# Kernel tuning notes

Measured on AMD Instinct MI355X. Metric: run time of the kernel, lower is better.

## Reference

```python
import jax, jax.numpy as jnp
import numpy as np

B, S, H, NH = 4, 2048, 512, 8
HD = H // NH  # head dim = 64


def setup_inputs() -> dict:
    key = jax.random.key(0)
    ks = jax.random.split(key, 12)
    f = lambda k, sh: jax.random.normal(k, sh, dtype=jnp.float32)
    w = lambda k: f(k, (H, H)) * 0.02  # Linear weight (out, in), torch-style
    return {
        "q": f(ks[0], (B, S, H)),
        "k": f(ks[1], (B, S, H)),
        "v": f(ks[2], (B, S, H)),
        "mask": jax.random.randint(ks[3], (B, S, S), 0, 2, dtype=jnp.int32),
        "Wq": w(ks[4]), "bq": jnp.zeros((H,), jnp.float32),
        "Wk": w(ks[5]), "bk": jnp.zeros((H,), jnp.float32),
        "Wv": w(ks[6]), "bv": jnp.zeros((H,), jnp.float32),
        "Wo": w(ks[7]), "bo": jnp.zeros((H,), jnp.float32),
    }


def reference(q, k, v, mask, Wq, bq, Wk, bk, Wv, bv, Wo, bo):
    b, s, h = q.shape
    scale = jnp.asarray(np.sqrt(HD), q.dtype)
    # QKV projections (torch Linear: x @ W.T + b), split into heads: b n s h
    def heads(x, W, bias):
        y = x @ W.T + bias
        return y.reshape(b, s, NH, HD).transpose(0, 2, 1, 3)
    Q = heads(q, Wq, bq)
    K = heads(k, Wk, bk)
    V = heads(v, Wv, bv)
    scores = jnp.einsum('bnsh,bnth->bnst', Q, K) / scale
    scores = jnp.where(mask[:, None, :, :] == 0, jnp.asarray(-1e9, scores.dtype), scores)
    attn = jax.nn.softmax(scores, axis=-1)
    # dropout is identity in eval mode
    out = jnp.einsum('bnst,bnth->bnsh', attn, V)
    out = out.transpose(0, 2, 1, 3).reshape(b, s, h)
    return out @ Wo.T + bo
```

## Files before the change

### kernel.cpp

```cpp
#include <hip/hip_runtime.h>
#include <cstdint>


typedef __bf16 bf16x8 __attribute__((ext_vector_type(8)));
typedef float  f32x4  __attribute__((ext_vector_type(4)));
typedef float  f32x16 __attribute__((ext_vector_type(16)));

#define MFMA16(a, b, c) __builtin_amdgcn_mfma_f32_16x16x32_bf16(a, b, c, 0, 0, 0)
#define MFMA32(a, b, c) __builtin_amdgcn_mfma_f32_32x32x16_bf16(a, b, c, 0, 0, 0)

__device__ __forceinline__ ushort f2bf(float f) {
  union { __bf16 h; ushort u; } v; v.h = (__bf16)f; return v.u;
}

typedef const __attribute__((address_space(1))) unsigned int* gas_u32;
typedef __attribute__((address_space(3))) unsigned int* las_u32;
__device__ __forceinline__ void gll16(const void* g, void* l) {
  __builtin_amdgcn_global_load_lds((gas_u32)g, (las_u32)l, 16, 0, 0);
}

__global__ __launch_bounds__(256) void cvt_bf16(
    const float* __restrict__ src, ushort* __restrict__ dst, int n4) {
  int i = blockIdx.x * 256 + threadIdx.x;
  int stride = gridDim.x * 256;
  for (; i < n4; i += stride) {
    float4 v = ((const float4*)src)[i];
    ushort4 o = { f2bf(v.x), f2bf(v.y), f2bf(v.z), f2bf(v.w) };
    ((ushort4*)dst)[i] = o;
  }
}

__global__ __launch_bounds__(256) void cvt_w(
    const float* __restrict__ w0, const float* __restrict__ w1,
    const float* __restrict__ w2, const float* __restrict__ w3,
    ushort* __restrict__ dst) {
  const float* src = (blockIdx.y == 0) ? w0 : (blockIdx.y == 1) ? w1
                   : (blockIdx.y == 2) ? w2 : w3;
  ushort* d = dst + (size_t)blockIdx.y * 262144;
  int i = blockIdx.x * 256 + threadIdx.x;
  for (int j = i; j < 65536; j += 16384) {
    float4 v = ((const float4*)src)[j];
    ushort4 o = { f2bf(v.x), f2bf(v.y), f2bf(v.z), f2bf(v.w) };
    ((ushort4*)d)[j] = o;
  }
}

__global__ __launch_bounds__(256) void mask_bits_kernel(
    const int* __restrict__ mask, unsigned long long* __restrict__ MB) {
  const int lane = threadIdx.x & 63;
  const int wv = (int)((blockIdx.x * 256 + threadIdx.x) >> 6);
  const size_t base = (size_t)wv * 64;
  for (int j = 0; j < 64; j += 4) {
    int v0 = mask[(base + j + 0) * 64 + lane];
    int v1 = mask[(base + j + 1) * 64 + lane];
    int v2 = mask[(base + j + 2) * 64 + lane];
    int v3 = mask[(base + j + 3) * 64 + lane];
    unsigned long long b0 = __ballot(v0 != 0), b1 = __ballot(v1 != 0);
    unsigned long long b2 = __ballot(v2 != 0), b3 = __ballot(v3 != 0);
    if (lane == 0) {
      MB[base + j] = b0; MB[base + j + 1] = b1;
      MB[base + j + 2] = b2; MB[base + j + 3] = b3;
    }
  }
}

template <int EPI>
__global__ __launch_bounds__(256) void gemm_bt16(
    const ushort* __restrict__ X, const ushort* __restrict__ W,
    const float* __restrict__ bias, void* __restrict__ Y, float scale) {
  __shared__ ushort As[64 * 64];
  __shared__ ushort Ws[128 * 64];
  const int tid = threadIdx.x, wv = tid >> 6, l = tid & 63;
  const int quad = l >> 4, ln = l & 15;
  const int m0 = blockIdx.x * 64, n0 = blockIdx.y * 128;
  const int wm = (wv & 1) * 32, wn = (wv >> 1) * 64;
  const int sr = l >> 3, sc = l & 7;
  f32x4 acc[2][4] = {};
  for (int kk = 0; kk < 512; kk += 64) {
#pragma unroll
    for (int i = 0; i < 2; ++i) {
      int row = wv * 16 + i * 8 + sr;
      gll16(X + (size_t)(m0 + row) * 512 + kk + ((sc ^ (row & 7)) * 8),
            As + (wv * 16 + i * 8) * 64);
    }
#pragma unroll
    for (int i = 0; i < 4; ++i) {
      int row = wv * 32 + i * 8 + sr;
      gll16(W + (size_t)(n0 + row) * 512 + kk + ((sc ^ (row & 7)) * 8),
            Ws + (wv * 32 + i * 8) * 64);
    }
    __syncthreads();
#pragma unroll
    for (int ks = 0; ks < 2; ++ks) {
      bf16x8 a[2], bw[4];
#pragma unroll
      for (int mt = 0; mt < 2; ++mt) {
        int row = wm + mt * 16 + ln;
        a[mt] = *(const bf16x8*)&As[row * 64 + (((ks * 4 + quad) ^ (row & 7)) * 8)];
      }
#pragma unroll
      for (int nt = 0; nt < 4; ++nt) {
        int row = wn + nt * 16 + ln;
        bw[nt] = *(const bf16x8*)&Ws[row * 64 + (((ks * 4 + quad) ^ (row & 7)) * 8)];
      }
#pragma unroll
      for (int mt = 0; mt < 2; ++mt)
#pragma unroll
        for (int nt = 0; nt < 4; ++nt)
          acc[mt][nt] = MFMA16(a[mt], bw[nt], acc[mt][nt]);
    }
    __syncthreads();
  }
  float bval[4];
#pragma unroll
  for (int nt = 0; nt < 4; ++nt) bval[nt] = bias[n0 + wn + nt * 16 + ln];

  if constexpr (EPI == 1) {
#pragma unroll
    for (int nt = 0; nt < 4; ++nt) {
      int row = wn + nt * 16 + ln;
#pragma unroll
      for (int mt = 0; mt < 2; ++mt) {
        int mbase = wm + mt * 16 + quad * 4;
        ushort4 pk;
        pk.x = f2bf(acc[mt][nt][0] + bval[nt]);
        pk.y = f2bf(acc[mt][nt][1] + bval[nt]);
        pk.z = f2bf(acc[mt][nt][2] + bval[nt]);
        pk.w = f2bf(acc[mt][nt][3] + bval[nt]);
        int col = ((mbase >> 3) ^ (row & 7)) * 8 + ((mbase >> 2) & 1) * 4;
        *(ushort4*)&Ws[row * 64 + col] = pk;
      }
    }
    __syncthreads();
#pragma unroll
    for (int i = 0; i < 4; ++i) {
      int c = tid + i * 256;
      int row = c >> 3, cs = c & 7;
      int cl = cs ^ (row & 7);
      uint4 d = *(const uint4*)&Ws[row * 64 + cs * 8];
      int n = n0 + row, m = m0 + cl * 8;
      int bb = m >> 11, s = m & 2047, h = n >> 6, hd = n & 63;
      *(uint4*)((ushort*)Y + ((size_t)((bb * 8 + h) * 64 + hd)) * 2048 + s) = d;
    }
  } else {
#pragma unroll
    for (int mt = 0; mt < 2; ++mt)
#pragma unroll
      for (int nt = 0; nt < 4; ++nt) {
        int n = n0 + wn + nt * 16 + ln;
#pragma unroll
        for (int r = 0; r < 4; ++r) {
          int m = m0 + wm + mt * 16 + quad * 4 + r;
          float val = (acc[mt][nt][r] + bval[nt]) * scale;
          if constexpr (EPI == 0) {
            int bb = m >> 11, s = m & 2047, h = n >> 6, hd = n & 63;
            ((ushort*)Y)[(((size_t)(bb * 8 + h) * 2048) + s) * 64 + hd] = f2bf(val);
          } else {
            ((float*)Y)[(size_t)m * 512 + n] = val;
          }
        }
      }
  }
}

__global__ __launch_bounds__(256, 4) void attn(
    const ushort* __restrict__ Qh, const ushort* __restrict__ Kh,
    const ushort* __restrict__ Vt, const unsigned long long* __restrict__ MB,
    ushort* __restrict__ O) {
  __shared__ ushort SMEM[16384];
  ushort* Ks = SMEM;
  ushort* Vs = SMEM + 8192;
  const int tid = threadIdx.x, wv = tid >> 6, lane = tid & 63;
  const int hs = lane >> 5, lq = lane & 31;
  const int qh = wv >> 1, kvh = wv & 1;
  const int bh = blockIdx.x, qb = blockIdx.y;
  const size_t hoff = (size_t)bh * 2048 * 64;
  const int q0 = qb * 64;
  const int qg = q0 + qh * 32 + lq;
  const int srK = lane >> 3, scK = lane & 7;
  const int srV = lane >> 4, scV = lane & 15;

  bf16x8 qf[4];
#pragma unroll
  for (int ki = 0; ki < 4; ++ki)
    qf[ki] = *(const bf16x8*)(Qh + hoff + (size_t)qg * 64 + ki * 16 + hs * 8);

  f32x16 po0 = {}, po1 = {};
  float l_own = 0.f;
  const unsigned long long* mrow = MB + ((size_t)(bh >> 3) * 2048 + qg) * 32;

  for (int it = 0; it < 16; ++it) {
    const int kv0 = it * 128;
#pragma unroll
    for (int i = 0; i < 4; ++i) {
      int row = wv * 32 + i * 8 + srK;
      gll16(Kh + hoff + (size_t)(kv0 + row) * 64 + ((scK ^ (row & 7)) * 8),
            Ks + (wv * 32 + i * 8) * 64);
      int rv = wv * 16 + i * 4 + srV;
      gll16(Vt + hoff + (size_t)rv * 2048 + kv0 + ((scV ^ (rv & 7)) * 8),
            Vs + (wv * 16 + i * 4) * 128);
    }
    unsigned long long mbw = mrow[it * 2 + kvh];
    __syncthreads();

#pragma unroll
    for (int ch = 0; ch < 2; ++ch) {
      const int kvb = kvh * 64 + ch * 32;
      f32x16 sc_ = {};
#pragma unroll
      for (int ki = 0; ki < 4; ++ki) {
        int row = kvb + lq;
        bf16x8 ak = *(const bf16x8*)&Ks[row * 64 + (((2 * ki + hs) ^ (row & 7)) * 8)];
        sc_ = MFMA32(ak, qf[ki], sc_);
      }
      uint pk[8];
      float psum = 0.f;
#pragma unroll
      for (int c = 0; c < 4; ++c) {
        unsigned nib = (unsigned)(mbw >> (ch * 32 + c * 8 + hs * 4)) & 0xFu;
        float p0 = (nib & 1u) ? exp2f(sc_[4 * c + 0]) : 0.f;
        float p1 = (nib & 2u) ? exp2f(sc_[4 * c + 1]) : 0.f;
        float p2 = (nib & 4u) ? exp2f(sc_[4 * c + 2]) : 0.f;
        float p3 = (nib & 8u) ? exp2f(sc_[4 * c + 3]) : 0.f;
        psum += (p0 + p1) + (p2 + p3);
        pk[2 * c + 0] = (uint)f2bf(p0) | ((uint)f2bf(p1) << 16);
        pk[2 * c + 1] = (uint)f2bf(p2) | ((uint)f2bf(p3) << 16);
      }
      l_own += psum;
      uint bx[4];
#pragma unroll
      for (int t2 = 0; t2 < 2; ++t2)
#pragma unroll
        for (int b2 = 0; b2 < 2; ++b2) {
          uint snd = hs ? pk[4 * t2 + b2] : pk[4 * t2 + 2 + b2];
          bx[t2 * 2 + b2] = (uint)__shfl_xor((int)snd, 32);
        }
#pragma unroll
      for (int t2 = 0; t2 < 2; ++t2) {
        union { uint u[4]; bf16x8 v; } bp;
        bp.u[0] = hs ? bx[2 * t2 + 0] : pk[4 * t2 + 0];
        bp.u[1] = hs ? bx[2 * t2 + 1] : pk[4 * t2 + 1];
        bp.u[2] = hs ? pk[4 * t2 + 2] : bx[2 * t2 + 0];
        bp.u[3] = hs ? pk[4 * t2 + 3] : bx[2 * t2 + 1];
#pragma unroll
        for (int m2 = 0; m2 < 2; ++m2) {
          int hd = m2 * 32 + lq;
          int gch = (kvb >> 3) + 2 * t2 + hs;
          bf16x8 av = *(const bf16x8*)&Vs[hd * 128 + ((gch ^ (hd & 7)) * 8)];
          if (m2 == 0) po0 = MFMA32(av, bp.v, po0);
          else         po1 = MFMA32(av, bp.v, po1);
        }
      }
    }
    __syncthreads();
  }

  l_own += __shfl_xor(l_own, 32);
  float* psh = (float*)Ks;
  float* lsh = (float*)Vs;
  ushort* Osh = Vs + 256;
  if (kvh == 1) {
#pragma unroll
    for (int i = 0; i < 16; ++i) psh[(qh * 32 + i) * 64 + lane] = po0[i];
#pragma unroll
    for (int i = 0; i < 16; ++i) psh[(qh * 32 + 16 + i) * 64 + lane] = po1[i];
    lsh[qh * 64 + lane] = l_own;
  }
  __syncthreads();
  if (kvh == 0) {
    float linv = 1.0f / (l_own + lsh[qh * 64 + lane]);
    int row = qh * 32 + lq;
#pragma unroll
    for (int m2 = 0; m2 < 2; ++m2) {
#pragma unroll
      for (int c = 0; c < 4; ++c)
#pragma unroll
        for (int b2 = 0; b2 < 2; ++b2) {
          int r = 4 * c + 2 * b2;
          float v0, v1;
          if (m2 == 0) {
            v0 = (po0[r] + psh[(qh * 32 + r) * 64 + lane]) * linv;
            v1 = (po0[r + 1] + psh[(qh * 32 + r + 1) * 64 + lane]) * linv;
          } else {
            v0 = (po1[r] + psh[(qh * 32 + 16 + r) * 64 + lane]) * linv;
            v1 = (po1[r + 1] + psh[(qh * 32 + 16 + r + 1) * 64 + lane]) * linv;
          }
          int hd = m2 * 32 + 8 * c + 4 * hs + 2 * b2;
          *(uint*)&Osh[row * 72 + hd] = (uint)f2bf(v0) | ((uint)f2bf(v1) << 16);
        }
    }
  }
  __syncthreads();
  for (int i = tid; i < 512; i += 256) {
    int row = i >> 3, cc = i & 7;
    uint4 d = *(const uint4*)&Osh[row * 72 + cc * 8];
    *(uint4*)(O + ((size_t)((bh >> 3) * 2048 + q0 + row)) * 512 +
              (bh & 7) * 64 + cc * 8) = d;
  }
}

extern "C" void kernel_launch(void* const* d_in, const int* in_sizes, int n_in,
                              void* d_out, int out_size, void* d_ws, size_t ws_size,
                              hipStream_t stream) {
  const float* q    = (const float*)d_in[0];
  const float* k    = (const float*)d_in[1];
  const float* v    = (const float*)d_in[2];
  const int*   mask = (const int*)d_in[3];
  const float* Wq   = (const float*)d_in[4];
  const float* bq   = (const float*)d_in[5];
  const float* Wk   = (const float*)d_in[6];
  const float* bk   = (const float*)d_in[7];
  const float* Wv   = (const float*)d_in[8];
  const float* bv   = (const float*)d_in[9];
  const float* Wo   = (const float*)d_in[10];
  const float* bo   = (const float*)d_in[11];
  float* out = (float*)d_out;

  uint8_t* ws = (uint8_t*)d_ws;
  const size_t MiB = 1u << 20;
  ushort* Xb = (ushort*)(ws + 0 * MiB);
  ushort* Qh = (ushort*)(ws + 8 * MiB);
  ushort* Kh = (ushort*)(ws + 16 * MiB);
  ushort* Vt = (ushort*)(ws + 24 * MiB);
  unsigned long long* MB = (unsigned long long*)(ws + 32 * MiB);
  ushort* Wb = (ushort*)(ws + 34 * MiB);

  cvt_w<<<dim3(64, 4), 256, 0, stream>>>(Wq, Wk, Wv, Wo, Wb);
  mask_bits_kernel<<<1024, 256, 0, stream>>>(mask, MB);

  cvt_bf16<<<1024, 256, 0, stream>>>(q, Xb, 1048576);
  gemm_bt16<0><<<dim3(128, 4), 256, 0, stream>>>(Xb, Wb, bq, Qh, 0.18033688011112042f);
  cvt_bf16<<<1024, 256, 0, stream>>>(k, Xb, 1048576);
  gemm_bt16<0><<<dim3(128, 4), 256, 0, stream>>>(Xb, Wb + 262144, bk, Kh, 1.0f);
  cvt_bf16<<<1024, 256, 0, stream>>>(v, Xb, 1048576);
  gemm_bt16<1><<<dim3(128, 4), 256, 0, stream>>>(Xb, Wb + 2 * 262144, bv, Vt, 1.0f);

  attn<<<dim3(32, 32), 256, 0, stream>>>(Qh, Kh, Vt, MB, Xb);
  gemm_bt16<2><<<dim3(128, 4), 256, 0, stream>>>(Xb, Wb + 3 * 262144, bo, out, 1.0f);
}
```

Measured before the change: 285.7 us.

## Fuse fp32-to-bf16 conversion into batched QKV GEMM and register-prefetch attention K/V

Drops the three separate activation conversion kernels. A single batched QKV GEMM launch (grid z=3) loads fp32 activations straight into LDS and converts them to bf16 when reading MFMA fragments. This removes three kernel launches and the round trip of the bf16 activation buffer through memory. The attention loop now double-buffers K/V tiles and mask words in registers, loading the next tile while computing the current one, in place of direct global-to-LDS loads followed by a barrier. The cost is higher register pressure and doubled fp32 LDS traffic in the GEMM. The LDS writes also lose the XOR swizzle on the store side, so they depend on the global address swizzle matching.

New measurement: 542.0 us. 1.9x slower.

```diff
diff --git a/kernel.cpp b/kernel.cpp
--- a/kernel.cpp
+++ b/kernel.cpp
@@ -17,17 +17,6 @@
 typedef __attribute__((address_space(3))) unsigned int* las_u32;
 __device__ __forceinline__ void gll16(const void* g, void* l) {
   __builtin_amdgcn_global_load_lds((gas_u32)g, (las_u32)l, 16, 0, 0);
-}
-
-__global__ __launch_bounds__(256) void cvt_bf16(
-    const float* __restrict__ src, ushort* __restrict__ dst, int n4) {
-  int i = blockIdx.x * 256 + threadIdx.x;
-  int stride = gridDim.x * 256;
-  for (; i < n4; i += stride) {
-    float4 v = ((const float4*)src)[i];
-    ushort4 o = { f2bf(v.x), f2bf(v.y), f2bf(v.z), f2bf(v.w) };
-    ((ushort4*)dst)[i] = o;
-  }
 }
 
 __global__ __launch_bounds__(256) void cvt_w(
@@ -64,29 +53,37 @@
   }
 }
 
-template <int EPI>
-__global__ __launch_bounds__(256) void gemm_bt16(
-    const ushort* __restrict__ X, const ushort* __restrict__ W,
-    const float* __restrict__ bias, void* __restrict__ Y, float scale) {
-  __shared__ ushort As[64 * 64];
+__global__ __launch_bounds__(256) void qkv_gemm(
+    const float* __restrict__ q, const float* __restrict__ k,
+    const float* __restrict__ v, const ushort* __restrict__ Wb,
+    const float* __restrict__ bq, const float* __restrict__ bk,
+    const float* __restrict__ bv, ushort* __restrict__ Qh,
+    ushort* __restrict__ Kh, ushort* __restrict__ Vt) {
+  __shared__ float  Asf[64 * 64];
   __shared__ ushort Ws[128 * 64];
+  const int z = blockIdx.z;
+  const float* X = (z == 0) ? q : (z == 1) ? k : v;
+  const ushort* W = Wb + (size_t)z * 262144;
+  const float* bias = (z == 0) ? bq : (z == 1) ? bk : bv;
+  const float scale = (z == 0) ? 0.18033688011112042f : 1.0f;
+  ushort* Y = (z == 0) ? Qh : (z == 1) ? Kh : Vt;
+
   const int tid = threadIdx.x, wv = tid >> 6, l = tid & 63;
   const int quad = l >> 4, ln = l & 15;
   const int m0 = blockIdx.x * 64, n0 = blockIdx.y * 128;
   const int wm = (wv & 1) * 32, wn = (wv >> 1) * 64;
-  const int sr = l >> 3, sc = l & 7;
+  const int srA = l >> 4, sA = l & 15, cA = sA >> 1, hA = sA & 1;
+  const int srW = l >> 3, scW = l & 7;
   f32x4 acc[2][4] = {};
+
   for (int kk = 0; kk < 512; kk += 64) {
 #pragma unroll
-    for (int i = 0; i < 2; ++i) {
-      int row = wv * 16 + i * 8 + sr;
-      gll16(X + (size_t)(m0 + row) * 512 + kk + ((sc ^ (row & 7)) * 8),
-            As + (wv * 16 + i * 8) * 64);
-    }
-#pragma unroll
     for (int i = 0; i < 4; ++i) {
-      int row = wv * 32 + i * 8 + sr;
-      gll16(W + (size_t)(n0 + row) * 512 + kk + ((sc ^ (row & 7)) * 8),
+      int rowa = wv * 16 + i * 4 + srA;
+      gll16(X + (size_t)(m0 + rowa) * 512 + kk + ((cA ^ (rowa & 7)) * 8 + hA * 4),
+            Asf + (wv * 16 + i * 4) * 64);
+      int roww = wv * 32 + i * 8 + srW;
+      gll16(W + (size_t)(n0 + roww) * 512 + kk + ((scW ^ (roww & 7)) * 8),
             Ws + (wv * 32 + i * 8) * 64);
     }
     __syncthreads();
@@ -96,7 +93,14 @@
 #pragma unroll
       for (int mt = 0; mt < 2; ++mt) {
         int row = wm + mt * 16 + ln;
-        a[mt] = *(const bf16x8*)&As[row * 64 + (((ks * 4 + quad) ^ (row & 7)) * 8)];
+        int p = (ks * 4 + quad) ^ (row & 7);
+        const float* ap = &Asf[row * 64 + p * 8];
+        f32x4 x0 = *(const f32x4*)ap;
+        f32x4 x1 = *(const f32x4*)(ap + 4);
+        bf16x8 t;
+#pragma unroll
+        for (int j = 0; j < 4; ++j) { t[j] = (__bf16)x0[j]; t[4 + j] = (__bf16)x1[j]; }
+        a[mt] = t;
       }
 #pragma unroll
       for (int nt = 0; nt < 4; ++nt) {
@@ -115,7 +119,7 @@
 #pragma unroll
   for (int nt = 0; nt < 4; ++nt) bval[nt] = bias[n0 + wn + nt * 16 + ln];
 
-  if constexpr (EPI == 1) {
+  if (z == 2) {
 #pragma unroll
     for (int nt = 0; nt < 4; ++nt) {
       int row = wn + nt * 16 + ln;
@@ -140,7 +144,7 @@
       uint4 d = *(const uint4*)&Ws[row * 64 + cs * 8];
       int n = n0 + row, m = m0 + cl * 8;
       int bb = m >> 11, s = m & 2047, h = n >> 6, hd = n & 63;
-      *(uint4*)((ushort*)Y + ((size_t)((bb * 8 + h) * 64 + hd)) * 2048 + s) = d;
+      *(uint4*)(Y + ((size_t)((bb * 8 + h) * 64 + hd)) * 2048 + s) = d;
     }
   } else {
 #pragma unroll
@@ -152,12 +156,8 @@
         for (int r = 0; r < 4; ++r) {
           int m = m0 + wm + mt * 16 + quad * 4 + r;
           float val = (acc[mt][nt][r] + bval[nt]) * scale;
-          if constexpr (EPI == 0) {
-            int bb = m >> 11, s = m & 2047, h = n >> 6, hd = n & 63;
-            ((ushort*)Y)[(((size_t)(bb * 8 + h) * 2048) + s) * 64 + hd] = f2bf(val);
-          } else {
-            ((float*)Y)[(size_t)m * 512 + n] = val;
-          }
+          int bb = m >> 11, s = m & 2047, h = n >> 6, hd = n & 63;
+          Y[(((size_t)(bb * 8 + h) * 2048) + s) * 64 + hd] = f2bf(val);
         }
       }
   }
@@ -179,30 +179,59 @@
   const int qg = q0 + qh * 32 + lq;
   const int srK = lane >> 3, scK = lane & 7;
   const int srV = lane >> 4, scV = lane & 15;
+  const ushort* Kbase = Kh + hoff;
+  const ushort* Vbase = Vt + hoff;
 
   bf16x8 qf[4];
 #pragma unroll
   for (int ki = 0; ki < 4; ++ki)
     qf[ki] = *(const bf16x8*)(Qh + hoff + (size_t)qg * 64 + ki * 16 + hs * 8);
+
+  int lK[4], lV[4];
+  size_t gK[4], gV[4];
+#pragma unroll
+  for (int i = 0; i < 4; ++i) {
+    int rowK = wv * 32 + i * 8 + srK;
+    gK[i] = (size_t)rowK * 64 + ((scK ^ (rowK & 7)) * 8);
+    lK[i] = rowK * 64 + scK * 8;
+    int rowV = wv * 16 + i * 4 + srV;
+    gV[i] = (size_t)rowV * 2048 + ((scV ^ (rowV & 7)) * 8);
+    lV[i] = rowV * 128 + scV * 8;
+  }
 
   f32x16 po0 = {}, po1 = {};
   float l_own = 0.f;
   const unsigned long long* mrow = MB + ((size_t)(bh >> 3) * 2048 + qg) * 32;
 
+  uint4 kr[2][4], vr[2][4];
+  unsigned long long mb[2];
+#pragma unroll
+  for (int i = 0; i < 4; ++i) {
+    kr[0][i] = *(const uint4*)(Kbase + gK[i]);
+    vr[0][i] = *(const uint4*)(Vbase + gV[i]);
+  }
+  mb[0] = mrow[kvh];
+
+#pragma unroll 2
   for (int it = 0; it < 16; ++it) {
-    const int kv0 = it * 128;
+    const int p = it & 1;
 #pragma unroll
     for (int i = 0; i < 4; ++i) {
-      int row = wv * 32 + i * 8 + srK;
-      gll16(Kh + hoff + (size_t)(kv0 + row) * 64 + ((scK ^ (row & 7)) * 8),
-            Ks + (wv * 32 + i * 8) * 64);
-      int rv = wv * 16 + i * 4 + srV;
-      gll16(Vt + hoff + (size_t)rv * 2048 + kv0 + ((scV ^ (rv & 7)) * 8),
-            Vs + (wv * 16 + i * 4) * 128);
-    }
-    unsigned long long mbw = mrow[it * 2 + kvh];
-    __syncthreads();
-
+      *(uint4*)&Ks[lK[i]] = kr[p][i];
+      *(uint4*)&Vs[lV[i]] = vr[p][i];
+    }
+    if (it < 15) {
+      const size_t kvo = (size_t)(it + 1) * 128;
+#pragma unroll
+      for (int i = 0; i < 4; ++i) {
+        kr[p ^ 1][i] = *(const uint4*)(Kbase + kvo * 64 + gK[i]);
+        vr[p ^ 1][i] = *(const uint4*)(Vbase + kvo + gV[i]);
+      }
+      mb[p ^ 1] = mrow[(it + 1) * 2 + kvh];
+    }
+    __syncthreads();
+
+    const unsigned long long mbw = mb[p];
 #pragma unroll
     for (int ch = 0; ch < 2; ++ch) {
       const int kvb = kvh * 64 + ch * 32;
@@ -297,6 +326,66 @@
     *(uint4*)(O + ((size_t)((bh >> 3) * 2048 + q0 + row)) * 512 +
               (bh & 7) * 64 + cc * 8) = d;
   }
+}
+
+__global__ __launch_bounds__(256) void out_gemm(
+    const ushort* __restrict__ X, const ushort* __restrict__ W,
+    const float* __restrict__ bias, float* __restrict__ Y) {
+  __shared__ ushort As[64 * 64];
+  __shared__ ushort Ws[128 * 64];
+  const int tid = threadIdx.x, wv = tid >> 6, l = tid & 63;
+  const int quad = l >> 4, ln = l & 15;
+  const int m0 = blockIdx.x * 64, n0 = blockIdx.y * 128;
+  const int wm = (wv & 1) * 32, wn = (wv >> 1) * 64;
+  const int sr = l >> 3, sc = l & 7;
+  f32x4 acc[2][4] = {};
+  for (int kk = 0; kk < 512; kk += 64) {
+#pragma unroll
+    for (int i = 0; i < 2; ++i) {
+      int row = wv * 16 + i * 8 + sr;
+      gll16(X + (size_t)(m0 + row) * 512 + kk + ((sc ^ (row & 7)) * 8),
+            As + (wv * 16 + i * 8) * 64);
+    }
+#pragma unroll
+    for (int i = 0; i < 4; ++i) {
+      int row = wv * 32 + i * 8 + sr;
+      gll16(W + (size_t)(n0 + row) * 512 + kk + ((sc ^ (row & 7)) * 8),
+            Ws + (wv * 32 + i * 8) * 64);
+    }
+    __syncthreads();
+#pragma unroll
+    for (int ks = 0; ks < 2; ++ks) {
+      bf16x8 a[2], bw[4];
+#pragma unroll
+      for (int mt = 0; mt < 2; ++mt) {
+        int row = wm + mt * 16 + ln;
+        a[mt] = *(const bf16x8*)&As[row * 64 + (((ks * 4 + quad) ^ (row & 7)) * 8)];
+      }
+#pragma unroll
+      for (int nt = 0; nt < 4; ++nt) {
+        int row = wn + nt * 16 + ln;
+        bw[nt] = *(const bf16x8*)&Ws[row * 64 + (((ks * 4 + quad) ^ (row & 7)) * 8)];
+      }
+#pragma unroll
+      for (int mt = 0; mt < 2; ++mt)
+#pragma unroll
+        for (int nt = 0; nt < 4; ++nt)
+          acc[mt][nt] = MFMA16(a[mt], bw[nt], acc[mt][nt]);
+    }
+    __syncthreads();
+  }
+#pragma unroll
+  for (int mt = 0; mt < 2; ++mt)
+#pragma unroll
+    for (int nt = 0; nt < 4; ++nt) {
+      int n = n0 + wn + nt * 16 + ln;
+      float bval = bias[n];
+#pragma unroll
+      for (int r = 0; r < 4; ++r) {
+        int m = m0 + wm + mt * 16 + quad * 4 + r;
+        Y[(size_t)m * 512 + n] = acc[mt][nt][r] + bval;
+      }
+    }
 }
 
 extern "C" void kernel_launch(void* const* d_in, const int* in_sizes, int n_in,
@@ -318,7 +407,7 @@
 
   uint8_t* ws = (uint8_t*)d_ws;
   const size_t MiB = 1u << 20;
-  ushort* Xb = (ushort*)(ws + 0 * MiB);
+  ushort* Oh = (ushort*)(ws + 0 * MiB);
   ushort* Qh = (ushort*)(ws + 8 * MiB);
   ushort* Kh = (ushort*)(ws + 16 * MiB);
   ushort* Vt = (ushort*)(ws + 24 * MiB);
@@ -327,14 +416,7 @@
 
   cvt_w<<<dim3(64, 4), 256, 0, stream>>>(Wq, Wk, Wv, Wo, Wb);
   mask_bits_kernel<<<1024, 256, 0, stream>>>(mask, MB);
-
-  cvt_bf16<<<1024, 256, 0, stream>>>(q, Xb, 1048576);
-  gemm_bt16<0><<<dim3(128, 4), 256, 0, stream>>>(Xb, Wb, bq, Qh, 0.18033688011112042f);
-  cvt_bf16<<<1024, 256, 0, stream>>>(k, Xb, 1048576);
-  gemm_bt16<0><<<dim3(128, 4), 256, 0, stream>>>(Xb, Wb + 262144, bk, Kh, 1.0f);
-  cvt_bf16<<<1024, 256, 0, stream>>>(v, Xb, 1048576);
-  gemm_bt16<1><<<dim3(128, 4), 256, 0, stream>>>(Xb, Wb + 2 * 262144, bv, Vt, 1.0f);
-
-  attn<<<dim3(32, 32), 256, 0, stream>>>(Qh, Kh, Vt, MB, Xb);
-  gemm_bt16<2><<<dim3(128, 4), 256, 0, stream>>>(Xb, Wb + 3 * 262144, bo, out, 1.0f);
-}
+  qkv_gemm<<<dim3(128, 4, 3), 256, 0, stream>>>(q, k, v, Wb, bq, bk, bv, Qh, Kh, Vt);
+  attn<<<dim3(32, 32), 256, 0, stream>>>(Qh, Kh, Vt, MB, Oh);
+  out_gemm<<<dim3(128, 4), 256, 0, stream>>>(Oh, Wb + 3 * 262144, bo, out);
+}
```
